# Kernel tuning notes

Measured on AMD Instinct MI355X. Metric: run time of the kernel, lower is better.

Reference implementation:

```python
import jax, jax.numpy as jnp
import numpy as np

B, H, S, D = 65536, 512, 256, 64  # batch, hidden_dim, memory_slots, slot_size


def setup_inputs() -> dict:
    key = jax.random.key(0)
    ks = jax.random.split(key, 8)
    scale = 1.0 / np.sqrt(H)
    return {
        "query": jax.random.normal(ks[0], (B, H), jnp.float32),
        "content": jax.random.normal(ks[1], (B, H), jnp.float32),
        "memory": jax.random.normal(ks[2], (S, D), jnp.float32),
        "memory_age": jax.random.uniform(ks[3], (S,), jnp.float32, 0.0, 30.0),
        "W_read": jax.random.normal(ks[4], (H, S), jnp.float32) * scale,
        "b_read": jnp.zeros((S,), jnp.float32),
        "W_write": jax.random.normal(ks[5], (H, S), jnp.float32) * scale,
        "b_write": jnp.zeros((S,), jnp.float32),
        "W_content": jax.random.normal(ks[6], (H, D), jnp.float32) * scale,
        "b_content": jnp.zeros((D,), jnp.float32),
    }


def reference(query, content, memory, memory_age,
              W_read, b_read, W_write, b_write, W_content, b_content):
    # ---- read: attention-based addressing over memory slots ----
    read_weights = jax.nn.softmax(query @ W_read + b_read, axis=-1)      # [B, S]
    read_content = read_weights @ memory                                  # [B, D]

    # ---- write: consolidation dynamics (vectorized per-slot EMA) ----
    write_weights = jax.nn.softmax(query @ W_write + b_write, axis=-1)   # [B, S]
    processed_content = content @ W_content + b_content                   # [B, D]
    w_mean = write_weights.mean(axis=0)                                    # [S]
    c_mean = processed_content.mean(axis=0)                                # [D]

    active = w_mean > 0.01                                                 # [S] bool
    consolidation = jax.nn.sigmoid(memory_age * 0.1)                       # [S]
    # effective blend factor; zero for inactive slots (slot left untouched)
    alpha = jnp.where(active, w_mean * consolidation, 0.0)[:, None]        # [S, 1]
    new_memory = (1.0 - alpha) * memory + alpha * c_mean[None, :]          # [S, D]
    new_age = memory_age + active.astype(memory_age.dtype)                 # [S]

    return read_content, new_memory, new_age
```

## Files before the change

kernel.cpp:

```cpp
#include <hip/hip_runtime.h>
#include <hip/hip_bf16.h>


typedef short short8 __attribute__((ext_vector_type(8)));
typedef float floatx4 __attribute__((ext_vector_type(4)));

#define H_DIM 512
#define BM 32

#define WS_WT    0
#define WS_MEMT  589824
#define WS_BFULL 622592
#define WS_WSUM  624896
#define WS_CSUM  625920

__device__ __forceinline__ unsigned short f2b(float f) {
  unsigned u = __float_as_uint(f);
  u += 0x7fffu + ((u >> 16) & 1u);
  return (unsigned short)(u >> 16);
}
__device__ __forceinline__ float b2f(unsigned short h) {
  return __uint_as_float(((unsigned)h) << 16);
}
__device__ __forceinline__ unsigned cvt2(float x, float y) {
  union { __hip_bfloat162 h; unsigned u; } c;
  c.h = __float22bfloat162_rn(make_float2(x, y));
  return c.u;
}
__device__ __forceinline__ void async16(const void* g, void* l) {
  __builtin_amdgcn_global_load_lds(
      (const __attribute__((address_space(1))) unsigned int*)g,
      (__attribute__((address_space(3))) unsigned int*)l, 16, 0, 0);
}

__global__ void drcn_init(const float* __restrict__ W_read, const float* __restrict__ W_write,
                          const float* __restrict__ W_content, const float* __restrict__ b_read,
                          const float* __restrict__ b_write, const float* __restrict__ b_content,
                          const float* __restrict__ memory,
                          unsigned short* __restrict__ Wt, unsigned short* __restrict__ memT,
                          float* __restrict__ bfull, float* __restrict__ w_sum,
                          float* __restrict__ c_sum) {
  int idx = blockIdx.x * 256 + threadIdx.x;
  if (idx < 294912) {
    int n = idx >> 9, k = idx & 511;
    float v;
    if (n < 256)      v = W_read[k * 256 + n];
    else if (n < 512) v = W_write[k * 256 + (n - 256)];
    else              v = W_content[k * 64 + (n - 512)];
    Wt[idx] = f2b(v);
  } else if (idx < 311296) {
    int i = idx - 294912;
    int d = i >> 8, s = i & 255;
    memT[i] = f2b(memory[s * 64 + d]);
  } else if (idx < 311872) {
    int n = idx - 311296;
    bfull[n] = (n < 256) ? b_read[n] : (n < 512 ? b_write[n - 256] : b_content[n - 512]);
  } else if (idx < 312192) {
    int i = idx - 311872;
    if (i < 256) w_sum[i] = 0.0f; else c_sum[i - 256] = 0.0f;
  }
}

__global__ __launch_bounds__(256, 2) void drcn_main(
    const float* __restrict__ query, const float* __restrict__ content,
    const unsigned short* __restrict__ Wt, const float* __restrict__ bfull,
    const unsigned short* __restrict__ memT, float* __restrict__ w_sum,
    float* __restrict__ c_sum, float* __restrict__ out) {
  __shared__ __align__(16) char smem[73728];
  unsigned short* lg = (unsigned short*)smem;
  float* cs = (float*)(smem + 37376);
  float* cp = (float*)(smem + 38400);

  const int t = threadIdx.x;
  const int wv = t >> 6;
  const int ln = t & 63;
  const int ln15 = ln & 15;
  const int quad = ln >> 4;
  const int m0 = blockIdx.x * BM;

  const char* wsrc = (const char*)Wt +
      (size_t)(((wv * 144 + (ln >> 2)) * 512 + (ln & 3) * 8) * 2);
  char* wbase = smem + wv * 9216;

  const float* qb[2]; const float* cb[2];
  #pragma unroll
  for (int mt = 0; mt < 2; mt++) {
    qb[mt] = query   + (size_t)(m0 + mt * 16 + ln15) * H_DIM + quad * 8;
    cb[mt] = content + (size_t)(m0 + mt * 16 + ln15) * H_DIM + quad * 8;
  }

  float bias[9];
  #pragma unroll
  for (int j = 0; j < 9; j++) bias[j] = bfull[(wv * 9 + j) * 16 + ln15];

  floatx4 acc[2][9];
  #pragma unroll
  for (int mt = 0; mt < 2; mt++)
    #pragma unroll
    for (int j = 0; j < 9; j++) {
      floatx4 z = {0.0f, 0.0f, 0.0f, 0.0f};
      acc[mt][j] = z;
    }

  float4 pq[2][2], pc[2][2];
  #pragma unroll
  for (int mt = 0; mt < 2; mt++) {
    pq[mt][0] = *(const float4*)(qb[mt]);
    pq[mt][1] = *(const float4*)(qb[mt] + 4);
    pc[mt][0] = *(const float4*)(cb[mt]);
    pc[mt][1] = *(const float4*)(cb[mt] + 4);
  }
  #pragma unroll
  for (int j = 0; j < 9; j++)
    async16(wsrc + j * 16384, wbase + j * 1024);

  #pragma unroll 2
  for (int it = 0; it < 16; ++it) {
    short8 aq[2], ac[2];
    #pragma unroll
    for (int mt = 0; mt < 2; mt++) {
      unsigned* p = (unsigned*)&aq[mt];
      p[0] = cvt2(pq[mt][0].x, pq[mt][0].y);
      p[1] = cvt2(pq[mt][0].z, pq[mt][0].w);
      p[2] = cvt2(pq[mt][1].x, pq[mt][1].y);
      p[3] = cvt2(pq[mt][1].z, pq[mt][1].w);
      unsigned* q = (unsigned*)&ac[mt];
      q[0] = cvt2(pc[mt][0].x, pc[mt][0].y);
      q[1] = cvt2(pc[mt][0].z, pc[mt][0].w);
      q[2] = cvt2(pc[mt][1].x, pc[mt][1].y);
      q[3] = cvt2(pc[mt][1].z, pc[mt][1].w);
    }
    asm volatile("s_waitcnt vmcnt(0)" ::: "memory");

    if (it < 15) {
      const int k1 = (it + 1) * 32;
      #pragma unroll
      for (int mt = 0; mt < 2; mt++) {
        pq[mt][0] = *(const float4*)(qb[mt] + k1);
        pq[mt][1] = *(const float4*)(qb[mt] + k1 + 4);
        pc[mt][0] = *(const float4*)(cb[mt] + k1);
        pc[mt][1] = *(const float4*)(cb[mt] + k1 + 4);
      }
      const char* ws2 = wsrc + (size_t)(it + 1) * 64;
      char* wd = smem + ((it + 1) & 1) * 36864 + wv * 9216;
      #pragma unroll
      for (int j = 0; j < 9; j++)
        async16(ws2 + j * 16384, wd + j * 1024);
    }

    const char* rb = smem + (it & 1) * 36864 + wv * 9216;
    #pragma unroll
    for (int j = 0; j < 9; j++) {
      short8 b = *(const short8*)(rb + j * 1024 + ln15 * 64 + quad * 16);
      const int nt = wv * 9 + j;
      #pragma unroll
      for (int mt = 0; mt < 2; mt++) {
        short8 a = (nt >= 32) ? ac[mt] : aq[mt];
        acc[mt][j] = __builtin_amdgcn_mfma_f32_16x16x32_bf16(a, b, acc[mt][j], 0, 0, 0);
      }
    }
  }
  __syncthreads();

  #pragma unroll
  for (int j = 0; j < 9; j++) {
    int n = (wv * 9 + j) * 16 + ln15;
    #pragma unroll
    for (int mt = 0; mt < 2; mt++) {
      #pragma unroll
      for (int r = 0; r < 4; r++) {
        int row = mt * 16 + quad * 4 + r;
        lg[row * 584 + n] = f2b(acc[mt][j][r] + bias[j]);
      }
    }
  }
  cs[t] = 0.0f;
  if (t < 64) cp[t] = 0.0f;
  __syncthreads();

  const int r = t >> 3, c = t & 7;
  unsigned short* lrow = lg + r * 584;

  {
    float v[32];
    #pragma unroll
    for (int ch = 0; ch < 4; ch++) {
      short8 u = *(const short8*)(lrow + c * 32 + ch * 8);
      #pragma unroll
      for (int e = 0; e < 8; e++) v[ch * 8 + e] = b2f((unsigned short)u[e]);
    }
    float mx = -3.0e38f;
    #pragma unroll
    for (int i = 0; i < 32; i++) mx = fmaxf(mx, v[i]);
    mx = fmaxf(mx, __shfl_xor(mx, 1));
    mx = fmaxf(mx, __shfl_xor(mx, 2));
    mx = fmaxf(mx, __shfl_xor(mx, 4));
    float sm = 0.0f;
    #pragma unroll
    for (int i = 0; i < 32; i++) { v[i] = __expf(v[i] - mx); sm += v[i]; }
    sm += __shfl_xor(sm, 1);
    sm += __shfl_xor(sm, 2);
    sm += __shfl_xor(sm, 4);
    float inv = 1.0f / sm;
    #pragma unroll
    for (int ch = 0; ch < 4; ch++) {
      short8 u;
      #pragma unroll
      for (int e = 0; e < 8; e++) u[e] = (short)f2b(v[ch * 8 + e] * inv);
      *(short8*)(lrow + c * 32 + ch * 8) = u;
    }
  }
  {
    float v[32];
    #pragma unroll
    for (int ch = 0; ch < 4; ch++) {
      short8 u = *(const short8*)(lrow + 256 + c * 32 + ch * 8);
      #pragma unroll
      for (int e = 0; e < 8; e++) v[ch * 8 + e] = b2f((unsigned short)u[e]);
    }
    float mx = -3.0e38f;
    #pragma unroll
    for (int i = 0; i < 32; i++) mx = fmaxf(mx, v[i]);
    mx = fmaxf(mx, __shfl_xor(mx, 1));
    mx = fmaxf(mx, __shfl_xor(mx, 2));
    mx = fmaxf(mx, __shfl_xor(mx, 4));
    float sm = 0.0f;
    #pragma unroll
    for (int i = 0; i < 32; i++) { v[i] = __expf(v[i] - mx); sm += v[i]; }
    sm += __shfl_xor(sm, 1);
    sm += __shfl_xor(sm, 2);
    sm += __shfl_xor(sm, 4);
    float inv = 1.0f / sm;
    #pragma unroll
    for (int i = 0; i < 32; i++) {
      float p = v[i] * inv;
      p += __shfl_xor(p, 8);
      p += __shfl_xor(p, 16);
      p += __shfl_xor(p, 32);
      v[i] = p;
    }
    if (ln < 8) {
      #pragma unroll
      for (int i = 0; i < 32; i++) atomicAdd(&cs[c * 32 + i], v[i]);
    }
  }
  {
    float v[8];
    short8 u = *(const short8*)(lrow + 512 + c * 8);
    #pragma unroll
    for (int e = 0; e < 8; e++) v[e] = b2f((unsigned short)u[e]);
    #pragma unroll
    for (int e = 0; e < 8; e++) {
      float p = v[e];
      p += __shfl_xor(p, 8);
      p += __shfl_xor(p, 16);
      p += __shfl_xor(p, 32);
      v[e] = p;
    }
    if (ln < 8) {
      #pragma unroll
      for (int e = 0; e < 8; e++) atomicAdd(&cp[c * 8 + e], v[e]);
    }
  }
  __syncthreads();

  {
    int mt = wv & 1, nd0 = (wv >> 1) * 2;
    floatx4 ra[2];
    floatx4 z = {0.0f, 0.0f, 0.0f, 0.0f};
    ra[0] = z; ra[1] = z;
    #pragma unroll
    for (int ks = 0; ks < 8; ks++) {
      int s0 = ks * 32 + quad * 8;
      short8 a = *(const short8*)(lg + (mt * 16 + ln15) * 584 + s0);
      #pragma unroll
      for (int dt = 0; dt < 2; dt++) {
        short8 b = *(const short8*)(memT + ((nd0 + dt) * 16 + ln15) * 256 + s0);
        ra[dt] = __builtin_amdgcn_mfma_f32_16x16x32_bf16(a, b, ra[dt], 0, 0, 0);
      }
    }
    #pragma unroll
    for (int dt = 0; dt < 2; dt++)
      #pragma unroll
      for (int rr = 0; rr < 4; rr++) {
        int orow = m0 + mt * 16 + quad * 4 + rr;
        out[(size_t)orow * 64 + (nd0 + dt) * 16 + ln15] = ra[dt][rr];
      }
  }

  atomicAdd(&w_sum[t], cs[t]);
  if (t < 64) atomicAdd(&c_sum[t], cp[t]);
}

__global__ void drcn_final(const float* __restrict__ memory, const float* __restrict__ age,
                           const float* __restrict__ w_sum, const float* __restrict__ c_sum,
                           float* __restrict__ out_mem, float* __restrict__ out_age) {
  int idx = blockIdx.x * 256 + threadIdx.x;
  int s = idx >> 6, d = idx & 63;
  float wm = w_sum[s] * (1.0f / 65536.0f);
  bool act = wm > 0.01f;
  float cons = 1.0f / (1.0f + __expf(-age[s] * 0.1f));
  float alpha = act ? wm * cons : 0.0f;
  float cm = c_sum[d] * (1.0f / 65536.0f);
  out_mem[idx] = (1.0f - alpha) * memory[idx] + alpha * cm;
  if (d == 0) out_age[s] = age[s] + (act ? 1.0f : 0.0f);
}

extern "C" void kernel_launch(void* const* d_in, const int* in_sizes, int n_in,
                              void* d_out, int out_size, void* d_ws, size_t ws_size,
                              hipStream_t stream) {
  (void)in_sizes; (void)n_in; (void)out_size; (void)ws_size;
  const float* query     = (const float*)d_in[0];
  const float* content   = (const float*)d_in[1];
  const float* memory    = (const float*)d_in[2];
  const float* mem_age   = (const float*)d_in[3];
  const float* W_read    = (const float*)d_in[4];
  const float* b_read    = (const float*)d_in[5];
  const float* W_write   = (const float*)d_in[6];
  const float* b_write   = (const float*)d_in[7];
  const float* W_content = (const float*)d_in[8];
  const float* b_content = (const float*)d_in[9];
  float* out = (float*)d_out;
  char* ws = (char*)d_ws;
  unsigned short* Wt   = (unsigned short*)(ws + WS_WT);
  unsigned short* memT = (unsigned short*)(ws + WS_MEMT);
  float* bfull = (float*)(ws + WS_BFULL);
  float* w_sum = (float*)(ws + WS_WSUM);
  float* c_sum = (float*)(ws + WS_CSUM);

  drcn_init<<<1220, 256, 0, stream>>>(W_read, W_write, W_content, b_read, b_write,
                                      b_content, memory, Wt, memT, bfull, w_sum, c_sum);
  drcn_main<<<2048, 256, 0, stream>>>(query, content, Wt, bfull, memT, w_sum, c_sum, out);
  drcn_final<<<64, 256, 0, stream>>>(memory, mem_age, w_sum, c_sum,
                                     out + 4194304, out + 4210688);
}
```

Before: 444.4 us.

## Stage activation tiles in LDS once and stream weights directly into registers

The kernel now loads the block's full query and content tiles up front, converts them to bf16 and stores them in a swizzled LDS layout, then reads A fragments from LDS each k-step. Weight B fragments are loaded straight from global memory into registers with a one-step register prefetch, replacing the double-buffered async global-to-LDS weight pipeline and its per-iteration vmcnt wait. LDS use drops from 72KB to 64KB. The cost is that the activation load is no longer overlapped with MFMA work, and the weight loads become per-lane 16-byte global reads that may be less coalesced and may stall at the MFMAs.

```diff
diff --git a/kernel.cpp b/kernel.cpp
--- a/kernel.cpp
+++ b/kernel.cpp
@@ -26,11 +26,6 @@
   union { __hip_bfloat162 h; unsigned u; } c;
   c.h = __float22bfloat162_rn(make_float2(x, y));
   return c.u;
-}
-__device__ __forceinline__ void async16(const void* g, void* l) {
-  __builtin_amdgcn_global_load_lds(
-      (const __attribute__((address_space(1))) unsigned int*)g,
-      (__attribute__((address_space(3))) unsigned int*)l, 16, 0, 0);
 }
 
 __global__ void drcn_init(const float* __restrict__ W_read, const float* __restrict__ W_write,
@@ -66,7 +61,7 @@
     const unsigned short* __restrict__ Wt, const float* __restrict__ bfull,
     const unsigned short* __restrict__ memT, float* __restrict__ w_sum,
     float* __restrict__ c_sum, float* __restrict__ out) {
-  __shared__ __align__(16) char smem[73728];
+  __shared__ __align__(16) char smem[65536];
   unsigned short* lg = (unsigned short*)smem;
   float* cs = (float*)(smem + 37376);
   float* cp = (float*)(smem + 38400);
@@ -78,21 +73,43 @@
   const int quad = ln >> 4;
   const int m0 = blockIdx.x * BM;
 
-  const char* wsrc = (const char*)Wt +
-      (size_t)(((wv * 144 + (ln >> 2)) * 512 + (ln & 3) * 8) * 2);
-  char* wbase = smem + wv * 9216;
-
-  const float* qb[2]; const float* cb[2];
+  const unsigned short* bp[9];
+  short8 breg[9];
   #pragma unroll
-  for (int mt = 0; mt < 2; mt++) {
-    qb[mt] = query   + (size_t)(m0 + mt * 16 + ln15) * H_DIM + quad * 8;
-    cb[mt] = content + (size_t)(m0 + mt * 16 + ln15) * H_DIM + quad * 8;
+  for (int j = 0; j < 9; j++) {
+    bp[j] = Wt + (size_t)(((wv * 9 + j) * 16 + ln15) * 512 + quad * 8);
+    breg[j] = *(const short8*)bp[j];
   }
 
   float bias[9];
   #pragma unroll
   for (int j = 0; j < 9; j++) bias[j] = bfull[(wv * 9 + j) * 16 + ln15];
 
+  {
+    const int row = t >> 3, jj = t & 7;
+    const float* qrow = query   + (size_t)(m0 + row) * H_DIM;
+    const float* crow = content + (size_t)(m0 + row) * H_DIM;
+    char* aqr = smem + row * 1024;
+    char* acr = smem + 32768 + row * 1024;
+    #pragma unroll
+    for (int i = 0; i < 8; i++) {
+      const int g = jj + i * 8;
+      const int sw = ((g ^ (row & 7)) << 4);
+      float4 f0 = *(const float4*)(qrow + g * 8);
+      float4 f1 = *(const float4*)(qrow + g * 8 + 4);
+      float4 g0 = *(const float4*)(crow + g * 8);
+      float4 g1 = *(const float4*)(crow + g * 8 + 4);
+      short8 s; unsigned* su = (unsigned*)&s;
+      su[0] = cvt2(f0.x, f0.y); su[1] = cvt2(f0.z, f0.w);
+      su[2] = cvt2(f1.x, f1.y); su[3] = cvt2(f1.z, f1.w);
+      *(short8*)(aqr + sw) = s;
+      short8 sc; unsigned* cu = (unsigned*)&sc;
+      cu[0] = cvt2(g0.x, g0.y); cu[1] = cvt2(g0.z, g0.w);
+      cu[2] = cvt2(g1.x, g1.y); cu[3] = cvt2(g1.z, g1.w);
+      *(short8*)(acr + sw) = sc;
+    }
+  }
+
   floatx4 acc[2][9];
   #pragma unroll
   for (int mt = 0; mt < 2; mt++)
@@ -102,62 +119,28 @@
       acc[mt][j] = z;
     }
 
-  float4 pq[2][2], pc[2][2];
-  #pragma unroll
-  for (int mt = 0; mt < 2; mt++) {
-    pq[mt][0] = *(const float4*)(qb[mt]);
-    pq[mt][1] = *(const float4*)(qb[mt] + 4);
-    pc[mt][0] = *(const float4*)(cb[mt]);
-    pc[mt][1] = *(const float4*)(cb[mt] + 4);
-  }
-  #pragma unroll
-  for (int j = 0; j < 9; j++)
-    async16(wsrc + j * 16384, wbase + j * 1024);
+  __syncthreads();
 
   #pragma unroll 2
   for (int it = 0; it < 16; ++it) {
     short8 aq[2], ac[2];
     #pragma unroll
     for (int mt = 0; mt < 2; mt++) {
-      unsigned* p = (unsigned*)&aq[mt];
-      p[0] = cvt2(pq[mt][0].x, pq[mt][0].y);
-      p[1] = cvt2(pq[mt][0].z, pq[mt][0].w);
-      p[2] = cvt2(pq[mt][1].x, pq[mt][1].y);
-      p[3] = cvt2(pq[mt][1].z, pq[mt][1].w);
-      unsigned* q = (unsigned*)&ac[mt];
-      q[0] = cvt2(pc[mt][0].x, pc[mt][0].y);
-      q[1] = cvt2(pc[mt][0].z, pc[mt][0].w);
-      q[2] = cvt2(pc[mt][1].x, pc[mt][1].y);
-      q[3] = cvt2(pc[mt][1].z, pc[mt][1].w);
-    }
-    asm volatile("s_waitcnt vmcnt(0)" ::: "memory");
-
-    if (it < 15) {
-      const int k1 = (it + 1) * 32;
-      #pragma unroll
-      for (int mt = 0; mt < 2; mt++) {
-        pq[mt][0] = *(const float4*)(qb[mt] + k1);
-        pq[mt][1] = *(const float4*)(qb[mt] + k1 + 4);
-        pc[mt][0] = *(const float4*)(cb[mt] + k1);
-        pc[mt][1] = *(const float4*)(cb[mt] + k1 + 4);
-      }
-      const char* ws2 = wsrc + (size_t)(it + 1) * 64;
-      char* wd = smem + ((it + 1) & 1) * 36864 + wv * 9216;
-      #pragma unroll
-      for (int j = 0; j < 9; j++)
-        async16(ws2 + j * 16384, wd + j * 1024);
-    }
-
-    const char* rb = smem + (it & 1) * 36864 + wv * 9216;
+      const int row = mt * 16 + ln15;
+      const int sw = row * 1024 + ((((it * 4 + quad) ^ (row & 7))) << 4);
+      aq[mt] = *(const short8*)(smem + sw);
+      ac[mt] = *(const short8*)(smem + 32768 + sw);
+    }
     #pragma unroll
     for (int j = 0; j < 9; j++) {
-      short8 b = *(const short8*)(rb + j * 1024 + ln15 * 64 + quad * 16);
       const int nt = wv * 9 + j;
       #pragma unroll
       for (int mt = 0; mt < 2; mt++) {
         short8 a = (nt >= 32) ? ac[mt] : aq[mt];
-        acc[mt][j] = __builtin_amdgcn_mfma_f32_16x16x32_bf16(a, b, acc[mt][j], 0, 0, 0);
+        acc[mt][j] = __builtin_amdgcn_mfma_f32_16x16x32_bf16(a, breg[j], acc[mt][j], 0, 0, 0);
       }
+      if (it < 15)
+        breg[j] = *(const short8*)(bp[j] + (it + 1) * 32);
     }
   }
   __syncthreads();
```

Result: faster. 420.4 us (-5.4%).
